# Performance work log

Measured on AMD Instinct MI355X. Metric: run time of the kernel, lower is better.

Reference implementation:

```python
import jax, jax.numpy as jnp
import numpy as np

N_NODES = 50000
N_EDGES = 625000
HIDDEN = 128
N_TYPES = 4


def setup_inputs() -> dict:
    key = jax.random.key(0)
    ks = jax.random.split(key, 10)
    s = 1.0 / np.sqrt(HIDDEN)
    return {
        "node_states": jax.random.normal(ks[0], (N_NODES, HIDDEN), dtype=jnp.float32),
        "edge_index": jax.random.randint(ks[1], (2, N_EDGES), 0, N_NODES, dtype=jnp.int64),
        "edge_type": jax.random.randint(ks[2], (N_EDGES,), 0, N_TYPES, dtype=jnp.int64),
        # per-edge-type Linear(hidden, hidden): weight [T, d, d] (torch: y = x @ W.T + b)
        "edge_W": jax.random.uniform(ks[3], (N_TYPES, HIDDEN, HIDDEN), jnp.float32, -s, s),
        "edge_b": jax.random.uniform(ks[4], (N_TYPES, HIDDEN), jnp.float32, -s, s),
        # GRUCell params (torch layout: [3d, d] for r|z|n gates)
        "w_ih": jax.random.uniform(ks[5], (3 * HIDDEN, HIDDEN), jnp.float32, -s, s),
        "w_hh": jax.random.uniform(ks[6], (3 * HIDDEN, HIDDEN), jnp.float32, -s, s),
        "b_ih": jax.random.uniform(ks[7], (3 * HIDDEN,), jnp.float32, -s, s),
        "b_hh": jax.random.uniform(ks[8], (3 * HIDDEN,), jnp.float32, -s, s),
    }


def reference(node_states, edge_index, edge_type, edge_W, edge_b, w_ih, w_hh, b_ih, b_hh):
    num_nodes = node_states.shape[0]
    src, dst = edge_index[0], edge_index[1]
    x_src = node_states[src]  # [E, d] gather of source states

    # per-edge-type linear; small fixed loop over edge types, masked accumulate
    msgs = jnp.zeros_like(x_src)
    for t in range(edge_W.shape[0]):
        m_t = x_src @ edge_W[t].T + edge_b[t]  # [E, d]
        msgs = msgs + jnp.where((edge_type == t)[:, None], m_t, 0.0)

    # scatter-sum messages into destination nodes
    agg = jax.ops.segment_sum(msgs, dst, num_segments=num_nodes)  # [N, d]

    # GRUCell(agg, node_states) — torch semantics
    gi = agg @ w_ih.T + b_ih          # [N, 3d]
    gh = node_states @ w_hh.T + b_hh  # [N, 3d]
    i_r, i_z, i_n = jnp.split(gi, 3, axis=1)
    h_r, h_z, h_n = jnp.split(gh, 3, axis=1)
    r = jax.nn.sigmoid(i_r + h_r)
    z = jax.nn.sigmoid(i_z + h_z)
    n = jnp.tanh(i_n + r * h_n)
    return (1.0 - z) * n + z * node_states
```

## Files before the change

kernel.cpp:

```cpp
#include <hip/hip_runtime.h>


typedef __attribute__((ext_vector_type(8))) short short8;
typedef __attribute__((ext_vector_type(4))) float floatx4;

#define HID 128
#define NTY 4

__device__ __forceinline__ unsigned short f2bf(float f) {
    unsigned int u = __float_as_uint(f);
    unsigned int r = (u + 0x7fffu + ((u >> 16) & 1u)) >> 16;
    return (unsigned short)r;
}
__device__ __forceinline__ float bf2f(unsigned int lo16) {
    return __uint_as_float(lo16 << 16);
}
__device__ __forceinline__ float frcp(float x) { return __builtin_amdgcn_rcpf(x); }

__device__ __forceinline__ void gload16(const unsigned short* g, unsigned short* l) {
    __builtin_amdgcn_global_load_lds(
        (const __attribute__((address_space(1))) unsigned int*)g,
        (__attribute__((address_space(3))) unsigned int*)l,
        16, 0, 0);
}


__global__ void prep_kernel(const float* __restrict__ h, unsigned short* __restrict__ hbf,
                            const float* __restrict__ W, unsigned short* __restrict__ Wc,
                            const float* __restrict__ w_ih, const float* __restrict__ w_hh,
                            unsigned short* __restrict__ Wg, float* __restrict__ bias4,
                            const float* __restrict__ b_ih, const float* __restrict__ b_hh,
                            int* __restrict__ deg4, int total4, int nb_cvt, int N4) {
    int b = blockIdx.x, tt = threadIdx.x;
    if (b < nb_cvt) {
        int i = b * 256 + tt;
        if (i < total4) {
            float4 v = ((const float4*)h)[i];
            uint2 o;
            o.x = (unsigned int)f2bf(v.x) | ((unsigned int)f2bf(v.y) << 16);
            o.y = (unsigned int)f2bf(v.z) | ((unsigned int)f2bf(v.w) << 16);
            ((uint2*)hbf)[i] = o;
        }
    } else if (b < nb_cvt + 256) {
        int idx = (b - nb_cvt) * 256 + tt;
        int j = idx >> 9, rem = idx & 511;
        int t = rem >> 7, k = rem & 127;
        Wc[idx] = f2bf(W[(t * HID + j) * HID + k]);
    } else if (b < nb_cvt + 768) {
        int idx = (b - nb_cvt - 256) * 256 + tt;
        int row = idx >> 8, k = idx & 255;
        int j = row >> 2, g = row & 3;
        float v = 0.0f;
        if (g == 0) v = (k < 128) ? w_ih[j * 128 + k]         : w_hh[j * 128 + (k - 128)];
        else if (g == 1) v = (k < 128) ? w_ih[(128 + j) * 128 + k] : w_hh[(128 + j) * 128 + (k - 128)];
        else if (g == 2) v = (k < 128) ? w_ih[(256 + j) * 128 + k] : 0.0f;
        else             v = (k < 128) ? 0.0f : w_hh[(256 + j) * 128 + (k - 128)];
        Wg[idx] = f2bf(v);
    } else if (b == nb_cvt + 768) {
        if (tt < 128) {
            float4 v;
            v.x = b_ih[tt] + b_hh[tt];
            v.y = b_ih[128 + tt] + b_hh[128 + tt];
            v.z = b_ih[256 + tt];
            v.w = b_hh[256 + tt];
            ((float4*)bias4)[tt] = v;
        }
    } else {
        int i = (b - nb_cvt - 769) * 256 + tt;
        if (i < N4) deg4[i] = 0;
    }
}


__global__ void hist4_kernel(const int* __restrict__ dst, const int* __restrict__ ety,
                             int* __restrict__ deg4, int E) {
    int e = blockIdx.x * blockDim.x + threadIdx.x;
    if (e < E) atomicAdd(&deg4[dst[e] * 4 + ety[e]], 1);
}

__global__ void scan_blocks4_kernel(const int* __restrict__ deg, int* __restrict__ rowptr,
                                    int* __restrict__ blocksum, int N4) {
    __shared__ int s[256];
    int t = threadIdx.x;
    int base = blockIdx.x * 1024 + t * 4;
    int v0 = 0, v1 = 0, v2 = 0, v3 = 0;
    if (base + 3 < N4) {
        v0 = deg[base]; v1 = deg[base + 1]; v2 = deg[base + 2]; v3 = deg[base + 3];
    } else {
        if (base < N4) v0 = deg[base];
        if (base + 1 < N4) v1 = deg[base + 1];
        if (base + 2 < N4) v2 = deg[base + 2];
    }
    int sum = v0 + v1 + v2 + v3;
    s[t] = sum;
    __syncthreads();
#pragma unroll
    for (int off = 1; off < 256; off <<= 1) {
        int x = (t >= off) ? s[t - off] : 0;
        __syncthreads();
        s[t] += x;
        __syncthreads();
    }
    int ex = s[t] - sum;
    if (base < N4) rowptr[base] = ex;
    if (base + 1 < N4) rowptr[base + 1] = ex + v0;
    if (base + 2 < N4) rowptr[base + 2] = ex + v0 + v1;
    if (base + 3 < N4) rowptr[base + 3] = ex + v0 + v1 + v2;
    if (t == 255) blocksum[blockIdx.x] = s[255];
}

__global__ void scan_top_kernel(const int* __restrict__ blocksum, int* __restrict__ blockoff, int nb) {
    __shared__ int s[256];
    int t = threadIdx.x;
    int v = (t < nb) ? blocksum[t] : 0;
    s[t] = v;
    __syncthreads();
#pragma unroll
    for (int off = 1; off < 256; off <<= 1) {
        int x = (t >= off) ? s[t - off] : 0;
        __syncthreads();
        s[t] += x;
        __syncthreads();
    }
    if (t < nb) blockoff[t] = s[t] - v;
}

__global__ void finalize4_kernel(int* __restrict__ rowptr, const int* __restrict__ blockoff,
                                 int* __restrict__ cursor, int N4, int E) {
    int i = blockIdx.x * blockDim.x + threadIdx.x;
    if (i >= N4) return;
    int r = rowptr[i] + blockoff[i >> 10];
    rowptr[i] = r;
    cursor[i] = r;
    if (i == 0) rowptr[N4] = E;
}

__global__ void fill4_kernel(const int* __restrict__ src, const int* __restrict__ dst,
                             const int* __restrict__ ety, int* __restrict__ cursor,
                             int* __restrict__ csr, int E) {
    int e = blockIdx.x * blockDim.x + threadIdx.x;
    if (e >= E) return;
    int pos = atomicAdd(&cursor[dst[e] * 4 + ety[e]], 1);
    csr[pos] = src[e];
}


__global__ void gather_s_kernel(const int* __restrict__ rowptr4, const int* __restrict__ csr,
                                const unsigned int* __restrict__ hbu,
                                float4* __restrict__ cnt4, unsigned int* __restrict__ Su, int N) {
    int w = blockIdx.x * (blockDim.x >> 6) + (threadIdx.x >> 6);
    if (w >= N) return;
    int lane = threadIdx.x & 63;
    int b0 = __builtin_amdgcn_readfirstlane(rowptr4[w * 4]);
    int b1 = __builtin_amdgcn_readfirstlane(rowptr4[w * 4 + 1]);
    int b2 = __builtin_amdgcn_readfirstlane(rowptr4[w * 4 + 2]);
    int b3 = __builtin_amdgcn_readfirstlane(rowptr4[w * 4 + 3]);
    int b4 = __builtin_amdgcn_readfirstlane(rowptr4[w * 4 + 4]);

    float s0 = 0.f, s1 = 0.f;
    float sn0[3], sn1[3];

    int e = b0;
    while (e + 8 <= b4) {
        int p[8];
        unsigned int u[8];
#pragma unroll
        for (int i = 0; i < 8; ++i) p[i] = csr[e + i];
#pragma unroll
        for (int i = 0; i < 8; ++i) u[i] = hbu[(size_t)p[i] * 64 + lane];
#pragma unroll
        for (int i = 0; i < 8; ++i) {
            int idx = e + i;
            if (idx == b1) { sn0[0] = s0; sn1[0] = s1; }
            if (idx == b2) { sn0[1] = s0; sn1[1] = s1; }
            if (idx == b3) { sn0[2] = s0; sn1[2] = s1; }
            s0 += bf2f(u[i] & 0xffffu);
            s1 += bf2f(u[i] >> 16);
        }
        e += 8;
    }
    {
        int rem = b4 - e;
        int p[7];
        unsigned int u[7];
#pragma unroll
        for (int i = 0; i < 7; ++i) if (i < rem) p[i] = csr[e + i];
#pragma unroll
        for (int i = 0; i < 7; ++i) if (i < rem) u[i] = hbu[(size_t)p[i] * 64 + lane];
#pragma unroll
        for (int i = 0; i < 7; ++i) {
            if (i < rem) {
                int idx = e + i;
                if (idx == b1) { sn0[0] = s0; sn1[0] = s1; }
                if (idx == b2) { sn0[1] = s0; sn1[1] = s1; }
                if (idx == b3) { sn0[2] = s0; sn1[2] = s1; }
                s0 += bf2f(u[i] & 0xffffu);
                s1 += bf2f(u[i] >> 16);
            }
        }
    }
    if (b1 == b4) { sn0[0] = s0; sn1[0] = s1; }
    if (b2 == b4) { sn0[1] = s0; sn1[1] = s1; }
    if (b3 == b4) { sn0[2] = s0; sn1[2] = s1; }

    size_t base = (size_t)w * 256 + lane;
    float a0, a1, p0 = 0.f, p1 = 0.f;
#pragma unroll
    for (int t = 0; t < 4; ++t) {
        float c0 = (t < 3) ? sn0[t] : s0;
        float c1 = (t < 3) ? sn1[t] : s1;
        a0 = c0 - p0; a1 = c1 - p1;
        p0 = c0; p1 = c1;
        Su[base + t * 64] = (unsigned int)f2bf(a0) | ((unsigned int)f2bf(a1) << 16);
    }
    if (lane == 0)
        cnt4[w] = make_float4((float)(b1 - b0), (float)(b2 - b1),
                              (float)(b3 - b2), (float)(b4 - b3));
}


__global__ __launch_bounds__(256, 3) void agg_gru(const unsigned short* __restrict__ S,
                                                  const unsigned short* __restrict__ Wc,
                                                  const unsigned short* __restrict__ Wg,
                                                  const unsigned short* __restrict__ hbf,
                                                  const float4* __restrict__ cnt4,
                                                  const float* __restrict__ eb,
                                                  const float4* __restrict__ bias4,
                                                  float* __restrict__ out, int M) {
    __shared__ __align__(16) unsigned char smem[49152];
    unsigned short* Sreg = (unsigned short*)smem;
    unsigned short* Hbt  = (unsigned short*)(smem + 8192);
    unsigned short* Wreg = (unsigned short*)(smem + 16384);
    unsigned short* Xag  = Sreg;
    float* OutsF = (float*)(smem + 16384);

    const int tid = threadIdx.x;
    const int m0 = blockIdx.x * 32;
    const int lane = tid & 63, w = tid >> 6;
    const int lm = lane & 15, quad = lane >> 4;

    floatx4 accA[2][2];
#pragma unroll
    for (int x = 0; x < 2; ++x)
#pragma unroll
        for (int y = 0; y < 2; ++y) accA[x][y] = (floatx4){0.f, 0.f, 0.f, 0.f};

#pragma unroll 1
    for (int c = 0; c < 4; ++c) {
#pragma unroll
        for (int i = 0; i < 2; ++i) {
            int k = w * 2 + i;
            int slot = k * 64 + lane;
            int row = slot >> 4, x = slot & 15;
            int grow = m0 + row; if (grow >= M) grow = M - 1;
            gload16(S + (size_t)grow * 512 + c * 128 + ((x ^ (row & 7)) << 3),
                    Sreg + k * 512);
        }
#pragma unroll
        for (int i = 0; i < 8; ++i) {
            int kk = w * 8 + i;
            int slot = kk * 64 + lane;
            int j = slot >> 4, x = slot & 15;
            gload16(Wc + (size_t)j * 512 + c * 128 + ((x ^ (j & 7)) << 3),
                    Wreg + kk * 512);
        }
        __syncthreads();
#pragma unroll
        for (int ss = 0; ss < 4; ++ss) {
            int g = ss * 4 + quad;
            short8 av[2], bw[2];
#pragma unroll
            for (int mi = 0; mi < 2; ++mi)
                av[mi] = *(const short8*)&Sreg[(mi * 16 + lm) * 128 + ((g ^ (lm & 7)) << 3)];
#pragma unroll
            for (int ni = 0; ni < 2; ++ni)
                bw[ni] = *(const short8*)&Wreg[(w * 32 + ni * 16 + lm) * 128 + ((g ^ (lm & 7)) << 3)];
#pragma unroll
            for (int mi = 0; mi < 2; ++mi)
#pragma unroll
                for (int ni = 0; ni < 2; ++ni)
                    accA[mi][ni] = __builtin_amdgcn_mfma_f32_16x16x32_bf16(av[mi], bw[ni], accA[mi][ni], 0, 0, 0);
        }
        __syncthreads();
    }

#pragma unroll
    for (int i = 0; i < 2; ++i) {
        int k = w * 2 + i;
        int slot = k * 64 + lane;
        int row = slot >> 4, x = slot & 15;
        int grow = m0 + row; if (grow >= M) grow = M - 1;
        gload16(hbf + (size_t)grow * HID + ((x ^ (row & 7)) << 3),
                Hbt + k * 512);
    }

    {
#pragma unroll
        for (int ni = 0; ni < 2; ++ni) {
            int j = w * 32 + ni * 16 + lm;
            float e0 = eb[j], e1 = eb[HID + j], e2 = eb[2 * HID + j], e3 = eb[3 * HID + j];
            int jg = j >> 3, jr = j & 7;
#pragma unroll
            for (int mi = 0; mi < 2; ++mi) {
#pragma unroll
                for (int r = 0; r < 4; ++r) {
                    int nl = mi * 16 + quad * 4 + r;
                    int gn = m0 + nl;
                    if (gn >= M) gn = M - 1;
                    float4 c4 = cnt4[gn];
                    float v = accA[mi][ni][r] + c4.x * e0 + c4.y * e1 + c4.z * e2 + c4.w * e3;
                    Xag[nl * 128 + ((jg ^ (nl & 7)) << 3) + jr] = f2bf(v);
                }
            }
        }
    }
    __syncthreads();

    float fin[4][2][2];

#pragma unroll 1
    for (int gc = 0; gc < 4; ++gc) {
        floatx4 acc2[2][2];
#pragma unroll
        for (int x = 0; x < 2; ++x)
#pragma unroll
            for (int y = 0; y < 2; ++y) acc2[x][y] = (floatx4){0.f, 0.f, 0.f, 0.f};

#pragma unroll 1
        for (int kc = 0; kc < 2; ++kc) {
#pragma unroll
            for (int i = 0; i < 8; ++i) {
                int kk = w * 8 + i;
                int slot = kk * 64 + lane;
                int rr = slot >> 4, x = slot & 15;
                gload16(Wg + (size_t)(gc * 128 + rr) * 256 + kc * 128 + ((x ^ (rr & 7)) << 3),
                        Wreg + kk * 512);
            }
            __syncthreads();
            const unsigned short* Bsrc = kc ? Hbt : Xag;
#pragma unroll
            for (int ss = 0; ss < 4; ++ss) {
                int g = ss * 4 + quad;
                short8 af[2], bfr[2];
#pragma unroll
                for (int mi2 = 0; mi2 < 2; ++mi2)
                    af[mi2] = *(const short8*)&Wreg[(w * 32 + mi2 * 16 + lm) * 128 + ((g ^ (lm & 7)) << 3)];
#pragma unroll
                for (int ni = 0; ni < 2; ++ni)
                    bfr[ni] = *(const short8*)&Bsrc[(ni * 16 + lm) * 128 + ((g ^ (lm & 7)) << 3)];
#pragma unroll
                for (int mi2 = 0; mi2 < 2; ++mi2)
#pragma unroll
                    for (int ni = 0; ni < 2; ++ni)
                        acc2[mi2][ni] = __builtin_amdgcn_mfma_f32_16x16x32_bf16(af[mi2], bfr[ni], acc2[mi2][ni], 0, 0, 0);
            }
            __syncthreads();
        }

#pragma unroll
        for (int mi2 = 0; mi2 < 2; ++mi2) {
            int j = gc * 32 + w * 8 + mi2 * 4 + quad;
            float4 bb = bias4[j];
            int jg = j >> 3, jr = j & 7;
#pragma unroll
            for (int ni = 0; ni < 2; ++ni) {
                int nl = ni * 16 + lm;
                float g0 = acc2[mi2][ni][0], g1 = acc2[mi2][ni][1];
                float g2 = acc2[mi2][ni][2], g3 = acc2[mi2][ni][3];
                float rr = frcp(1.f + __expf(-(g0 + bb.x)));
                float zz = frcp(1.f + __expf(-(g1 + bb.y)));
                float aa = g2 + bb.z + rr * (g3 + bb.w);
                float nn = 1.f - 2.f * frcp(1.f + __expf(2.f * aa));
                float hv = bf2f((unsigned int)Hbt[nl * 128 + ((jg ^ (nl & 7)) << 3) + jr]);
                fin[gc][mi2][ni] = nn + zz * (hv - nn);
            }
        }
    }
    __syncthreads();

#pragma unroll
    for (int gc = 0; gc < 4; ++gc) {
#pragma unroll
        for (int mi2 = 0; mi2 < 2; ++mi2) {
            int j = gc * 32 + w * 8 + mi2 * 4 + quad;
            int gq = j >> 2, jr = j & 3;
#pragma unroll
            for (int ni = 0; ni < 2; ++ni) {
                int nl = ni * 16 + lm;
                OutsF[nl * 128 + ((gq ^ (nl & 7)) << 2) + jr] = fin[gc][mi2][ni];
            }
        }
    }
    __syncthreads();

    {
        int row = tid >> 3;
        int cb = (tid & 7) * 16;
        int node = m0 + row;
        if (node < M) {
            float* dstp = out + (size_t)node * HID + cb;
#pragma unroll
            for (int i = 0; i < 4; ++i) {
                int gq = (cb >> 2) + i;
                *(float4*)(dstp + i * 4) = *(const float4*)&OutsF[row * 128 + ((gq ^ (row & 7)) << 2)];
            }
        }
    }
}


extern "C" void kernel_launch(void* const* d_in, const int* in_sizes, int n_in,
                              void* d_out, int out_size, void* d_ws, size_t ws_size,
                              hipStream_t stream) {
    const float* node_states = (const float*)d_in[0];
    const int*   edge_index  = (const int*)d_in[1];
    const int*   edge_type   = (const int*)d_in[2];
    const float* edge_W      = (const float*)d_in[3];
    const float* edge_b      = (const float*)d_in[4];
    const float* w_ih        = (const float*)d_in[5];
    const float* w_hh        = (const float*)d_in[6];
    const float* b_ih        = (const float*)d_in[7];
    const float* b_hh        = (const float*)d_in[8];

    const int M = in_sizes[0] / HID;
    const int E = in_sizes[1] / 2;
    const int N4 = M * 4;
    const int* src = edge_index;
    const int* dst = edge_index + E;

    char* ws = (char*)d_ws;
    size_t off = 0;
    unsigned short* hbf   = (unsigned short*)(ws + off); off += (size_t)M * HID * 2;
    float*          bias4 = (float*)(ws + off);          off += (size_t)128 * 4 * 4;
    unsigned short* S     = (unsigned short*)(ws + off); off += (size_t)M * 512 * 2;
    unsigned short* Wcat  = (unsigned short*)(ws + off); off += (size_t)128 * 512 * 2;
    unsigned short* Wgru  = (unsigned short*)(ws + off); off += (size_t)512 * 256 * 2;
    float*          cnt4  = (float*)(ws + off);          off += (size_t)M * 4 * 4;
    int* deg4     = (int*)(ws + off); off += (size_t)N4 * 4;
    int* rowptr4  = (int*)(ws + off); off += (size_t)(N4 + 1) * 4;
    int* cursor4  = (int*)(ws + off); off += (size_t)N4 * 4;
    int* blocksum = (int*)(ws + off); off += 256 * 4;
    int* blockoff = (int*)(ws + off); off += 256 * 4;
    int* csr      = (int*)(ws + off); off += (size_t)E * 4;

    const int total4 = M * HID / 4;
    const int nb_cvt = (total4 + 255) / 256;
    const int nb_zero = (N4 + 255) / 256;
    const int nb_scan = (N4 + 1023) / 1024;

    prep_kernel<<<nb_cvt + 769 + nb_zero, 256, 0, stream>>>(
        node_states, hbf, edge_W, Wcat, w_ih, w_hh, Wgru, bias4, b_ih, b_hh,
        deg4, total4, nb_cvt, N4);

    hist4_kernel<<<(E + 255) / 256, 256, 0, stream>>>(dst, edge_type, deg4, E);
    scan_blocks4_kernel<<<nb_scan, 256, 0, stream>>>(deg4, rowptr4, blocksum, N4);
    scan_top_kernel<<<1, 256, 0, stream>>>(blocksum, blockoff, nb_scan);
    finalize4_kernel<<<(N4 + 255) / 256, 256, 0, stream>>>(rowptr4, blockoff, cursor4, N4, E);
    fill4_kernel<<<(E + 255) / 256, 256, 0, stream>>>(src, dst, edge_type, cursor4, csr, E);

    gather_s_kernel<<<(M + 3) / 4, 256, 0, stream>>>(rowptr4, csr, (const unsigned int*)hbf,
                                                     (float4*)cnt4, (unsigned int*)S, M);

    agg_gru<<<(M + 31) / 32, 256, 0, stream>>>(S, Wcat, Wgru, hbf, (const float4*)cnt4,
                                               edge_b, (const float4*)bias4, (float*)d_out, M);
}
```

Measured before the change: 243.8 us.

## Merge histogram into prep kernel and fold top-level scan into finalize

Zeroes the degree array with hipMemsetAsync so the edge histogram atomics can run inside the prep/conversion kernel, removing one launch. Every finalize block now redundantly scans the small block-sum array in shared memory instead of a separate single-block scan kernel writing block offsets, removing another launch. The goal is less launch overhead and fewer serial kernel boundaries, at the cost of a memset call and redundant per-block scan work.

```diff
diff --git a/kernel.cpp b/kernel.cpp
--- a/kernel.cpp
+++ b/kernel.cpp
@@ -25,12 +25,13 @@
 }
 
 
-__global__ void prep_kernel(const float* __restrict__ h, unsigned short* __restrict__ hbf,
-                            const float* __restrict__ W, unsigned short* __restrict__ Wc,
-                            const float* __restrict__ w_ih, const float* __restrict__ w_hh,
-                            unsigned short* __restrict__ Wg, float* __restrict__ bias4,
-                            const float* __restrict__ b_ih, const float* __restrict__ b_hh,
-                            int* __restrict__ deg4, int total4, int nb_cvt, int N4) {
+__global__ void prep_hist_kernel(const float* __restrict__ h, unsigned short* __restrict__ hbf,
+                                 const float* __restrict__ W, unsigned short* __restrict__ Wc,
+                                 const float* __restrict__ w_ih, const float* __restrict__ w_hh,
+                                 unsigned short* __restrict__ Wg, float* __restrict__ bias4,
+                                 const float* __restrict__ b_ih, const float* __restrict__ b_hh,
+                                 const int* __restrict__ dst, const int* __restrict__ ety,
+                                 int* __restrict__ deg4, int total4, int nb_cvt, int E) {
     int b = blockIdx.x, tt = threadIdx.x;
     if (b < nb_cvt) {
         int i = b * 256 + tt;
@@ -66,17 +67,11 @@
             ((float4*)bias4)[tt] = v;
         }
     } else {
-        int i = (b - nb_cvt - 769) * 256 + tt;
-        if (i < N4) deg4[i] = 0;
-    }
-}
-
-
-__global__ void hist4_kernel(const int* __restrict__ dst, const int* __restrict__ ety,
-                             int* __restrict__ deg4, int E) {
-    int e = blockIdx.x * blockDim.x + threadIdx.x;
-    if (e < E) atomicAdd(&deg4[dst[e] * 4 + ety[e]], 1);
-}
+        int e = (b - nb_cvt - 769) * 256 + tt;
+        if (e < E) atomicAdd(&deg4[dst[e] * 4 + ety[e]], 1);
+    }
+}
+
 
 __global__ void scan_blocks4_kernel(const int* __restrict__ deg, int* __restrict__ rowptr,
                                     int* __restrict__ blocksum, int N4) {
@@ -109,7 +104,9 @@
     if (t == 255) blocksum[blockIdx.x] = s[255];
 }
 
-__global__ void scan_top_kernel(const int* __restrict__ blocksum, int* __restrict__ blockoff, int nb) {
+
+__global__ void finalize_top_kernel(const int* __restrict__ blocksum, int* __restrict__ rowptr,
+                                    int* __restrict__ cursor, int N4, int E, int nb) {
     __shared__ int s[256];
     int t = threadIdx.x;
     int v = (t < nb) ? blocksum[t] : 0;
@@ -122,16 +119,14 @@
         s[t] += x;
         __syncthreads();
     }
-    if (t < nb) blockoff[t] = s[t] - v;
-}
-
-__global__ void finalize4_kernel(int* __restrict__ rowptr, const int* __restrict__ blockoff,
-                                 int* __restrict__ cursor, int N4, int E) {
-    int i = blockIdx.x * blockDim.x + threadIdx.x;
-    if (i >= N4) return;
-    int r = rowptr[i] + blockoff[i >> 10];
-    rowptr[i] = r;
-    cursor[i] = r;
+    int i = blockIdx.x * blockDim.x + t;
+    if (i < N4) {
+        int c = i >> 10;
+        int off0 = (c == 0) ? 0 : s[c - 1];
+        int r = rowptr[i] + off0;
+        rowptr[i] = r;
+        cursor[i] = r;
+    }
     if (i == 0) rowptr[N4] = E;
 }
 
@@ -440,22 +435,24 @@
     int* rowptr4  = (int*)(ws + off); off += (size_t)(N4 + 1) * 4;
     int* cursor4  = (int*)(ws + off); off += (size_t)N4 * 4;
     int* blocksum = (int*)(ws + off); off += 256 * 4;
-    int* blockoff = (int*)(ws + off); off += 256 * 4;
     int* csr      = (int*)(ws + off); off += (size_t)E * 4;
 
     const int total4 = M * HID / 4;
     const int nb_cvt = (total4 + 255) / 256;
-    const int nb_zero = (N4 + 255) / 256;
+    const int nb_hist = (E + 255) / 256;
     const int nb_scan = (N4 + 1023) / 1024;
 
-    prep_kernel<<<nb_cvt + 769 + nb_zero, 256, 0, stream>>>(
+    hipMemsetAsync(deg4, 0, (size_t)N4 * 4, stream);
+
+    prep_hist_kernel<<<nb_cvt + 769 + nb_hist, 256, 0, stream>>>(
         node_states, hbf, edge_W, Wcat, w_ih, w_hh, Wgru, bias4, b_ih, b_hh,
-        deg4, total4, nb_cvt, N4);
-
-    hist4_kernel<<<(E + 255) / 256, 256, 0, stream>>>(dst, edge_type, deg4, E);
+        dst, edge_type, deg4, total4, nb_cvt, E);
+
     scan_blocks4_kernel<<<nb_scan, 256, 0, stream>>>(deg4, rowptr4, blocksum, N4);
-    scan_top_kernel<<<1, 256, 0, stream>>>(blocksum, blockoff, nb_scan);
-    finalize4_kernel<<<(N4 + 255) / 256, 256, 0, stream>>>(rowptr4, blockoff, cursor4, N4, E);
+
+    finalize_top_kernel<<<(N4 + 255) / 256, 256, 0, stream>>>(blocksum, rowptr4, cursor4,
+                                                              N4, E, nb_scan);
+
     fill4_kernel<<<(E + 255) / 256, 256, 0, stream>>>(src, dst, edge_type, cursor4, csr, E);
 
     gather_s_kernel<<<(M + 3) / 4, 256, 0, stream>>>(rowptr4, csr, (const unsigned int*)hbf,
```

New measurement: 241.1 us. Within noise of the previous version (-1.1%).
